# Kernel optimization log

Measured on AMD Instinct MI355X. Metric: run time of the kernel, lower is better.

## Reference

```python
import jax, jax.numpy as jnp
import numpy as np

TEMPERATURE = 0.1
EPS = 1e-12  # matches F.normalize eps clamp


def setup_inputs() -> dict:
    key = jax.random.key(0)
    k1, k2 = jax.random.split(key)
    B, D = 4096, 1024
    z1 = jax.random.normal(k1, (B, D), dtype=jnp.float32)
    z2 = jax.random.normal(k2, (B, D), dtype=jnp.float32)
    return {"z1": z1, "z2": z2}


def reference(z1, z2):
    B = z1.shape[0]
    # L2-normalize rows (F.normalize dim=1, eps clamp)
    n1 = z1 / jnp.maximum(jnp.linalg.norm(z1, axis=1, keepdims=True), EPS)
    n2 = z2 / jnp.maximum(jnp.linalg.norm(z2, axis=1, keepdims=True), EPS)
    reps = jnp.concatenate([n1, n2], axis=0)  # [2B, D]
    # Rows are unit-norm, so cosine similarity == dot product -> one GEMM
    sim = (reps @ reps.T) / TEMPERATURE  # [2B, 2B]
    # positives: diag offsets +B and -B
    pos = jnp.concatenate([jnp.diagonal(sim, B), jnp.diagonal(sim, -B)])  # [2B]
    # logits row i = [pos_i, sim[i, j != i]]. logsumexp over that set =
    # logaddexp(pos_i, logsumexp over the row with the main diagonal removed).
    eye = jnp.eye(2 * B, dtype=bool)
    masked = jnp.where(eye, -jnp.inf, sim)
    lse_neg = jax.scipy.special.logsumexp(masked, axis=1)  # [2B]
    lse = jnp.logaddexp(pos, lse_neg)
    # CrossEntropyLoss with labels==0 -> mean(lse - logit_0) = mean(lse - pos)
    return jnp.mean(lse - pos)
```

## Files before the change

kernel.cpp:

```cpp
#include <hip/hip_runtime.h>

#define D_DIM 1024
#define B_HALF 4096
#define NROWS 8192
#define INV_T8 (10.0f / 256.0f)
#define NKT 32
#define NBIG 512
#define NBLK 576

typedef float floatx4 __attribute__((ext_vector_type(4)));

#define MFMA8 __builtin_amdgcn_mfma_f32_16x16x32_fp8_fp8
#define AS1 const __attribute__((address_space(1))) unsigned int*
#define AS3 __attribute__((address_space(3))) unsigned int*

__global__ __launch_bounds__(256) void normalize_kernel(
    const float* __restrict__ z1, const float* __restrict__ z2,
    unsigned char* __restrict__ R8, float* __restrict__ S)
{
    const int tid = threadIdx.x;
    const int lane = tid & 63;
    const int row = blockIdx.x * 4 + (tid >> 6);
    const float* src = (row < B_HALF) ? (z1 + (size_t)row * D_DIM)
                                      : (z2 + (size_t)(row - B_HALF) * D_DIM);
    const float4* s4 = (const float4*)src;
    float4 v0 = s4[lane], v1 = s4[64 + lane], v2 = s4[128 + lane], v3 = s4[192 + lane];
    if (lane == 0) S[row] = 0.0f;
    float ss = v0.x*v0.x + v0.y*v0.y + v0.z*v0.z + v0.w*v0.w
             + v1.x*v1.x + v1.y*v1.y + v1.z*v1.z + v1.w*v1.w
             + v2.x*v2.x + v2.y*v2.y + v2.z*v2.z + v2.w*v2.w
             + v3.x*v3.x + v3.y*v3.y + v3.z*v3.z + v3.w*v3.w;
    ss += __shfl_xor(ss, 1);
    ss += __shfl_xor(ss, 2);
    ss += __shfl_xor(ss, 4);
    ss += __shfl_xor(ss, 8);
    ss += __shfl_xor(ss, 16);
    ss += __shfl_xor(ss, 32);
    float scale = 16.0f / fmaxf(sqrtf(ss), 1e-12f);
    int* dst = (int*)(R8 + (size_t)row * D_DIM);
    float4 vv[4] = {v0, v1, v2, v3};
    #pragma unroll
    for (int i = 0; i < 4; ++i) {
        int w = __builtin_amdgcn_cvt_pk_fp8_f32(vv[i].x * scale, vv[i].y * scale, 0, 0);
        w = __builtin_amdgcn_cvt_pk_fp8_f32(vv[i].z * scale, vv[i].w * scale, w, 1);
        dst[i * 64 + lane] = w;
    }
}

__global__ __launch_bounds__(512, 2) void gemm_lse_kernel(
    const unsigned char* __restrict__ R8,
    float* __restrict__ S, float* __restrict__ pos)
{
    __shared__ unsigned char lds8[2][2][256 * 32];

    const int tid = threadIdx.x;
    const int wave = tid >> 6, lane = tid & 63;
    const int lm = lane & 15, lq = lane >> 4;
    const int wm = wave >> 2, wn = wave & 3;

    if (blockIdx.x < NBIG) {
        int t = blockIdx.x;
        #pragma unroll
        for (int i = 0; i < 16; ++i) {
            const int h = 32 * i - (i * (i - 1)) / 2 + 16;
            if (t >= h) ++t;
        }
        int rt = 0;
        while (t >= 32 - rt) { t -= 32 - rt; ++rt; }
        const int ct = rt + t;
        const bool isDiag = (rt == ct);
        const int row0 = rt * 256, col0 = ct * 256;

        const unsigned char* __restrict__ gA = R8 + (size_t)row0 * D_DIM;
        const unsigned char* __restrict__ gB = R8 + (size_t)col0 * D_DIM;

        floatx4 acc[8][4] = {};

#define BSTAGE(d, kk) \
        { __builtin_amdgcn_global_load_lds( \
            (AS1)(gA + (size_t)(wave * 32 + (lane >> 1)) * D_DIM + (kk) + (lane & 1) * 16), \
            (AS3)(&lds8[d][0][wave * 1024]), 16, 0, 0); \
          __builtin_amdgcn_global_load_lds( \
            (AS1)(gB + (size_t)(wave * 32 + (lane >> 1)) * D_DIM + (kk) + (lane & 1) * 16), \
            (AS3)(&lds8[d][1][wave * 1024]), 16, 0, 0); }

        BSTAGE(0, 0)
        asm volatile("s_waitcnt vmcnt(0)" ::: "memory");
        __builtin_amdgcn_s_barrier();

        for (int kt = 0; kt < NKT; ++kt) {
            const int buf = kt & 1;
            const unsigned char* As = &lds8[buf][0][0];
            const unsigned char* Bs = &lds8[buf][1][0];
            if (kt + 1 < NKT) BSTAGE(buf ^ 1, (kt + 1) * 32)

            long af[8], bf[4];
            #pragma unroll
            for (int mi = 0; mi < 8; ++mi)
                af[mi] = *(const long*)(As + (wm * 128 + mi * 16 + lm) * 32 + lq * 8);
            #pragma unroll
            for (int ni = 0; ni < 4; ++ni)
                bf[ni] = *(const long*)(Bs + (wn * 64 + ni * 16 + lm) * 32 + lq * 8);

            __builtin_amdgcn_s_setprio(1);
            #pragma unroll
            for (int mi = 0; mi < 8; ++mi)
                #pragma unroll
                for (int ni = 0; ni < 4; ++ni)
                    acc[mi][ni] = MFMA8(af[mi], bf[ni], acc[mi][ni], 0, 0, 0);
            __builtin_amdgcn_s_setprio(0);

            asm volatile("s_waitcnt vmcnt(0)" ::: "memory");
            __builtin_amdgcn_s_barrier();
        }

        float* rowsum = (float*)&lds8[0][0][0];
        float* colsum = rowsum + 4 * 256;
        float ecol[4] = {0.0f, 0.0f, 0.0f, 0.0f};
        #pragma unroll
        for (int mi = 0; mi < 8; ++mi) {
            const int rloc = wm * 128 + mi * 16 + lq * 4;
            #pragma unroll
            for (int reg = 0; reg < 4; ++reg) {
                const int gr = row0 + rloc + reg;
                float esum = 0.0f;
                #pragma unroll
                for (int ni = 0; ni < 4; ++ni) {
                    const int gc = col0 + wn * 64 + ni * 16 + lm;
                    float s = acc[mi][ni][reg] * INV_T8;
                    if (gc == gr + B_HALF) { pos[gr] = s; pos[gc] = s; }
                    float e = (gc == gr) ? 0.0f : __expf(s);
                    esum += e;
                    ecol[ni] += e;
                }
                esum += __shfl_xor(esum, 1);
                esum += __shfl_xor(esum, 2);
                esum += __shfl_xor(esum, 4);
                esum += __shfl_xor(esum, 8);
                if (lm == 0) rowsum[wn * 256 + rloc + reg] = esum;
            }
        }
        #pragma unroll
        for (int ni = 0; ni < 4; ++ni) {
            ecol[ni] += __shfl_xor(ecol[ni], 16);
            ecol[ni] += __shfl_xor(ecol[ni], 32);
        }
        if (lq == 0 && !isDiag) {
            #pragma unroll
            for (int ni = 0; ni < 4; ++ni)
                colsum[wm * 256 + wn * 64 + ni * 16 + lm] = ecol[ni];
        }
        __syncthreads();
        if (tid < 256) {
            float rs = rowsum[tid] + rowsum[256 + tid]
                     + rowsum[512 + tid] + rowsum[768 + tid];
            atomicAdd(&S[row0 + tid], rs);
            if (!isDiag) {
                float cs = colsum[tid] + colsum[256 + tid];
                atomicAdd(&S[col0 + tid], cs);
            }
        }
    } else {
        const int s = blockIdx.x - NBIG;
        const int p = s >> 2, qr = (s >> 1) & 1, qc = s & 1;
        const int row0 = (2 * p + qr) * 128;
        const int col0 = (2 * p + 32 + qc) * 128;

        const unsigned char* __restrict__ gA = R8 + (size_t)row0 * D_DIM;
        const unsigned char* __restrict__ gB = R8 + (size_t)col0 * D_DIM;

        floatx4 acc[4][2] = {};

#define SSTAGE(d, kk) \
        { const int m_ = wave >> 2; \
          const unsigned char* g_ = m_ ? gB : gA; \
          const int w_ = wave & 3; \
          __builtin_amdgcn_global_load_lds( \
            (AS1)(g_ + (size_t)(w_ * 32 + (lane >> 1)) * D_DIM + (kk) + (lane & 1) * 16), \
            (AS3)(&lds8[d][m_][w_ * 1024]), 16, 0, 0); }

        SSTAGE(0, 0)
        asm volatile("s_waitcnt vmcnt(0)" ::: "memory");
        __builtin_amdgcn_s_barrier();

        for (int kt = 0; kt < NKT; ++kt) {
            const int buf = kt & 1;
            const unsigned char* As = &lds8[buf][0][0];
            const unsigned char* Bs = &lds8[buf][1][0];
            if (kt + 1 < NKT) SSTAGE(buf ^ 1, (kt + 1) * 32)

            long af[4], bf[2];
            #pragma unroll
            for (int mi = 0; mi < 4; ++mi)
                af[mi] = *(const long*)(As + (wm * 64 + mi * 16 + lm) * 32 + lq * 8);
            #pragma unroll
            for (int ni = 0; ni < 2; ++ni)
                bf[ni] = *(const long*)(Bs + (wn * 32 + ni * 16 + lm) * 32 + lq * 8);

            __builtin_amdgcn_s_setprio(1);
            #pragma unroll
            for (int mi = 0; mi < 4; ++mi)
                #pragma unroll
                for (int ni = 0; ni < 2; ++ni)
                    acc[mi][ni] = MFMA8(af[mi], bf[ni], acc[mi][ni], 0, 0, 0);
            __builtin_amdgcn_s_setprio(0);

            asm volatile("s_waitcnt vmcnt(0)" ::: "memory");
            __builtin_amdgcn_s_barrier();
        }

        float* rowsum = (float*)&lds8[0][0][0];
        float* colsum = rowsum + 4 * 128;
        float ecol[2] = {0.0f, 0.0f};
        #pragma unroll
        for (int mi = 0; mi < 4; ++mi) {
            const int rloc = wm * 64 + mi * 16 + lq * 4;
            #pragma unroll
            for (int reg = 0; reg < 4; ++reg) {
                const int gr = row0 + rloc + reg;
                float esum = 0.0f;
                #pragma unroll
                for (int ni = 0; ni < 2; ++ni) {
                    const int gc = col0 + wn * 32 + ni * 16 + lm;
                    float s = acc[mi][ni][reg] * INV_T8;
                    if (gc == gr + B_HALF) { pos[gr] = s; pos[gc] = s; }
                    float e = __expf(s);
                    esum += e;
                    ecol[ni] += e;
                }
                esum += __shfl_xor(esum, 1);
                esum += __shfl_xor(esum, 2);
                esum += __shfl_xor(esum, 4);
                esum += __shfl_xor(esum, 8);
                if (lm == 0) rowsum[wn * 128 + rloc + reg] = esum;
            }
        }
        #pragma unroll
        for (int ni = 0; ni < 2; ++ni) {
            ecol[ni] += __shfl_xor(ecol[ni], 16);
            ecol[ni] += __shfl_xor(ecol[ni], 32);
        }
        if (lq == 0) {
            #pragma unroll
            for (int ni = 0; ni < 2; ++ni)
                colsum[wm * 128 + wn * 32 + ni * 16 + lm] = ecol[ni];
        }
        __syncthreads();
        if (tid < 128) {
            float rs = rowsum[tid] + rowsum[128 + tid]
                     + rowsum[256 + tid] + rowsum[384 + tid];
            atomicAdd(&S[row0 + tid], rs);
            float cs = colsum[tid] + colsum[128 + tid];
            atomicAdd(&S[col0 + tid], cs);
        }
    }
}

__global__ __launch_bounds__(1024) void finalize_kernel(
    const float* __restrict__ S, const float* __restrict__ pos,
    float* __restrict__ out)
{
    const int tid = threadIdx.x;
    float local = 0.0f;
    #pragma unroll
    for (int i = 0; i < 8; ++i) {
        const int r = i * 1024 + tid;
        local += log1pf(S[r] * __expf(-pos[r]));
    }
    #pragma unroll
    for (int off = 32; off > 0; off >>= 1) local += __shfl_down(local, off);
    __shared__ float ws[16];
    if ((tid & 63) == 0) ws[tid >> 6] = local;
    __syncthreads();
    if (tid == 0) {
        float tot = 0.0f;
        #pragma unroll
        for (int i = 0; i < 16; ++i) tot += ws[i];
        out[0] = tot * (1.0f / 8192.0f);
    }
}

extern "C" void kernel_launch(void* const* d_in, const int* in_sizes, int n_in,
                              void* d_out, int out_size, void* d_ws, size_t ws_size,
                              hipStream_t stream)
{
    const float* z1 = (const float*)d_in[0];
    const float* z2 = (const float*)d_in[1];
    float* out = (float*)d_out;
    char* ws = (char*)d_ws;
    unsigned char* R8 = (unsigned char*)ws;
    float* pos = (float*)(ws + (size_t)8 * 1024 * 1024);
    float* S   = (float*)(ws + (size_t)8 * 1024 * 1024 + 65536);

    normalize_kernel<<<2048, 256, 0, stream>>>(z1, z2, R8, S);
    gemm_lse_kernel<<<NBLK, 512, 0, stream>>>(R8, S, pos);
    finalize_kernel<<<1, 1024, 0, stream>>>(S, pos, out);
}
```

Before: 184.0 us.

## Double K-tile depth to 64 and XOR-swizzle LDS layout for fp8 GEMM

Each main-loop iteration now covers K=64 instead of K=32, which halves the number of iterations and barriers and issues two MFMAs per accumulator per step. The LDS staging tiles are widened to 64 bytes per row and the global_load_lds writes use an XOR swizzle on the 16-byte chunk index. The fragment reads apply the matching swizzle to avoid LDS bank conflicts. In exchange, LDS use doubles to 64 KB per block and more fragment registers are live, which may limit occupancy at two blocks per CU.

```diff
diff --git a/kernel.cpp b/kernel.cpp
--- a/kernel.cpp
+++ b/kernel.cpp
@@ -4,7 +4,7 @@
 #define B_HALF 4096
 #define NROWS 8192
 #define INV_T8 (10.0f / 256.0f)
-#define NKT 32
+#define NKT64 16
 #define NBIG 512
 #define NBLK 576
 
@@ -51,12 +51,17 @@
     const unsigned char* __restrict__ R8,
     float* __restrict__ S, float* __restrict__ pos)
 {
-    __shared__ unsigned char lds8[2][2][256 * 32];
+    __shared__ unsigned char lds8[2][2][256 * 64];
 
     const int tid = threadIdx.x;
     const int wave = tid >> 6, lane = tid & 63;
     const int lm = lane & 15, lq = lane >> 4;
     const int wm = wave >> 2, wn = wave & 3;
+    const int sRow = lane >> 2;
+    const int sCol = (lane & 3) ^ ((sRow >> 1) & 3);
+    const int gswz = ((lm >> 1) & 3) << 1;
+    const int sk0 = (lq ^ gswz) * 8;
+    const int sk1 = ((4 + lq) ^ gswz) * 8;
 
     if (blockIdx.x < NBIG) {
         int t = blockIdx.x;
@@ -77,37 +82,46 @@
         floatx4 acc[8][4] = {};
 
 #define BSTAGE(d, kk) \
-        { __builtin_amdgcn_global_load_lds( \
-            (AS1)(gA + (size_t)(wave * 32 + (lane >> 1)) * D_DIM + (kk) + (lane & 1) * 16), \
-            (AS3)(&lds8[d][0][wave * 1024]), 16, 0, 0); \
-          __builtin_amdgcn_global_load_lds( \
-            (AS1)(gB + (size_t)(wave * 32 + (lane >> 1)) * D_DIM + (kk) + (lane & 1) * 16), \
-            (AS3)(&lds8[d][1][wave * 1024]), 16, 0, 0); }
+        { _Pragma("unroll") for (int i = 0; i < 2; ++i) { \
+            __builtin_amdgcn_global_load_lds( \
+              (AS1)(gA + (size_t)(wave * 32 + i * 16 + sRow) * D_DIM + (kk) + sCol * 16), \
+              (AS3)(&lds8[d][0][(wave * 32 + i * 16) * 64]), 16, 0, 0); \
+            __builtin_amdgcn_global_load_lds( \
+              (AS1)(gB + (size_t)(wave * 32 + i * 16 + sRow) * D_DIM + (kk) + sCol * 16), \
+              (AS3)(&lds8[d][1][(wave * 32 + i * 16) * 64]), 16, 0, 0); } }
 
         BSTAGE(0, 0)
         asm volatile("s_waitcnt vmcnt(0)" ::: "memory");
         __builtin_amdgcn_s_barrier();
 
-        for (int kt = 0; kt < NKT; ++kt) {
+        for (int kt = 0; kt < NKT64; ++kt) {
             const int buf = kt & 1;
             const unsigned char* As = &lds8[buf][0][0];
             const unsigned char* Bs = &lds8[buf][1][0];
-            if (kt + 1 < NKT) BSTAGE(buf ^ 1, (kt + 1) * 32)
-
-            long af[8], bf[4];
-            #pragma unroll
-            for (int mi = 0; mi < 8; ++mi)
-                af[mi] = *(const long*)(As + (wm * 128 + mi * 16 + lm) * 32 + lq * 8);
-            #pragma unroll
-            for (int ni = 0; ni < 4; ++ni)
-                bf[ni] = *(const long*)(Bs + (wn * 64 + ni * 16 + lm) * 32 + lq * 8);
+            if (kt + 1 < NKT64) BSTAGE(buf ^ 1, (kt + 1) * 64)
+
+            long af[8][2], bf[4][2];
+            #pragma unroll
+            for (int mi = 0; mi < 8; ++mi) {
+                const int r = (wm * 128 + mi * 16 + lm) * 64;
+                af[mi][0] = *(const long*)(As + r + sk0);
+                af[mi][1] = *(const long*)(As + r + sk1);
+            }
+            #pragma unroll
+            for (int ni = 0; ni < 4; ++ni) {
+                const int r = (wn * 64 + ni * 16 + lm) * 64;
+                bf[ni][0] = *(const long*)(Bs + r + sk0);
+                bf[ni][1] = *(const long*)(Bs + r + sk1);
+            }
 
             __builtin_amdgcn_s_setprio(1);
             #pragma unroll
             for (int mi = 0; mi < 8; ++mi)
                 #pragma unroll
-                for (int ni = 0; ni < 4; ++ni)
-                    acc[mi][ni] = MFMA8(af[mi], bf[ni], acc[mi][ni], 0, 0, 0);
+                for (int ni = 0; ni < 4; ++ni) {
+                    acc[mi][ni] = MFMA8(af[mi][0], bf[ni][0], acc[mi][ni], 0, 0, 0);
+                    acc[mi][ni] = MFMA8(af[mi][1], bf[ni][1], acc[mi][ni], 0, 0, 0);
+                }
             __builtin_amdgcn_s_setprio(0);
 
             asm volatile("s_waitcnt vmcnt(0)" ::: "memory");
@@ -175,34 +189,43 @@
         { const int m_ = wave >> 2; \
           const unsigned char* g_ = m_ ? gB : gA; \
           const int w_ = wave & 3; \
-          __builtin_amdgcn_global_load_lds( \
-            (AS1)(g_ + (size_t)(w_ * 32 + (lane >> 1)) * D_DIM + (kk) + (lane & 1) * 16), \
-            (AS3)(&lds8[d][m_][w_ * 1024]), 16, 0, 0); }
+          _Pragma("unroll") for (int i = 0; i < 2; ++i) { \
+            __builtin_amdgcn_global_load_lds( \
+              (AS1)(g_ + (size_t)(w_ * 32 + i * 16 + sRow) * D_DIM + (kk) + sCol * 16), \
+              (AS3)(&lds8[d][m_][(w_ * 32 + i * 16) * 64]), 16, 0, 0); } }
 
         SSTAGE(0, 0)
         asm volatile("s_waitcnt vmcnt(0)" ::: "memory");
         __builtin_amdgcn_s_barrier();
 
-        for (int kt = 0; kt < NKT; ++kt) {
+        for (int kt = 0; kt < NKT64; ++kt) {
             const int buf = kt & 1;
             const unsigned char* As = &lds8[buf][0][0];
             const unsigned char* Bs = &lds8[buf][1][0];
-            if (kt + 1 < NKT) SSTAGE(buf ^ 1, (kt + 1) * 32)
-
-            long af[4], bf[2];
-            #pragma unroll
-            for (int mi = 0; mi < 4; ++mi)
-                af[mi] = *(const long*)(As + (wm * 64 + mi * 16 + lm) * 32 + lq * 8);
-            #pragma unroll
-            for (int ni = 0; ni < 2; ++ni)
-                bf[ni] = *(const long*)(Bs + (wn * 32 + ni * 16 + lm) * 32 + lq * 8);
+            if (kt + 1 < NKT64) SSTAGE(buf ^ 1, (kt + 1) * 64)
+
+            long af[4][2], bf[2][2];
+            #pragma unroll
+            for (int mi = 0; mi < 4; ++mi) {
+                const int r = (wm * 64 + mi * 16 + lm) * 64;
+                af[mi][0] = *(const long*)(As + r + sk0);
+                af[mi][1] = *(const long*)(As + r + sk1);
+            }
+            #pragma unroll
+            for (int ni = 0; ni < 2; ++ni) {
+                const int r = (wn * 32 + ni * 16 + lm) * 64;
+                bf[ni][0] = *(const long*)(Bs + r + sk0);
+                bf[ni][1] = *(const long*)(Bs + r + sk1);
+            }
 
             __builtin_amdgcn_s_setprio(1);
             #pragma unroll
             for (int mi = 0; mi < 4; ++mi)
                 #pragma unroll
-                for (int ni = 0; ni < 2; ++ni)
-                    acc[mi][ni] = MFMA8(af[mi], bf[ni], acc[mi][ni], 0, 0, 0);
+                for (int ni = 0; ni < 2; ++ni) {
+                    acc[mi][ni] = MFMA8(af[mi][0], bf[ni][0], acc[mi][ni], 0, 0, 0);
+                    acc[mi][ni] = MFMA8(af[mi][1], bf[ni][1], acc[mi][ni], 0, 0, 0);
+                }
             __builtin_amdgcn_s_setprio(0);
 
             asm volatile("s_waitcnt vmcnt(0)" ::: "memory");
```

New measurement: 163.0 us. -11.4%, faster.
